# Performance work log

Measured on AMD Instinct MI355X. Metric: run time of the kernel, lower is better.

Reference implementation:

```python
import jax, jax.numpy as jnp
import numpy as np

N, R, B, D, E, P = 100000, 8, 4, 64, 2000000, 500000


def rgcn_conv(x, edge_index, edge_type, comp, basis, root, bias):
    # PyG RGCNConv with basis decomposition and default aggr='mean':
    # per relation r: h_v = mean_{(u->v), type r} x_u ; out_v += h_v @ W_r
    # W_r = sum_b comp[r,b] * basis[b]
    W = jnp.einsum('rb,bio->rio', comp, basis)            # [R, in, out]
    src, dst = edge_index[0], edge_index[1]
    seg = dst * R + edge_type                              # per-(node, relation) segment
    msg = x[src]                                           # [E, in] gather
    sums = jax.ops.segment_sum(msg, seg, num_segments=N * R)
    cnt = jax.ops.segment_sum(jnp.ones((src.shape[0],), x.dtype), seg, num_segments=N * R)
    mean = sums / jnp.maximum(cnt, 1.0)[:, None]           # empty segment -> 0, like PyG
    mean = mean.reshape(N, R, -1)                          # [N, R, in]
    out = jnp.einsum('nri,rio->no', mean, W)
    out = out + x @ root + bias                            # root (self) transform + bias
    return out


def setup_inputs() -> dict:
    key = jax.random.key(0)
    ks = jax.random.split(key, 16)
    s = 0.1
    return {
        'edge_index': jax.random.randint(ks[0], (2, E), 0, N),
        'edge_type': jax.random.randint(ks[1], (E,), 0, R),
        'edge_pairs': jax.random.randint(ks[2], (P, 2), 0, N),
        'node_emb': jax.random.normal(ks[3], (N, D), jnp.float32),
        'comp1': jax.random.normal(ks[4], (R, B), jnp.float32) * s,
        'basis1': jax.random.normal(ks[5], (B, D, D), jnp.float32) * s,
        'root1': jax.random.normal(ks[6], (D, D), jnp.float32) * s,
        'bias1': jnp.zeros((D,), jnp.float32),
        'comp2': jax.random.normal(ks[7], (R, B), jnp.float32) * s,
        'basis2': jax.random.normal(ks[8], (B, D, D), jnp.float32) * s,
        'root2': jax.random.normal(ks[9], (D, D), jnp.float32) * s,
        'bias2': jnp.zeros((D,), jnp.float32),
        'W1': jax.random.normal(ks[10], (2 * D, D), jnp.float32) * s,
        'b1': jnp.zeros((D,), jnp.float32),
        'W2': jax.random.normal(ks[11], (D, 1), jnp.float32) * s,
        'b2': jnp.zeros((1,), jnp.float32),
    }


def reference(edge_index, edge_type, edge_pairs, node_emb, comp1, basis1, root1, bias1,
              comp2, basis2, root2, bias2, W1, b1, W2, b2):
    # encode (eval mode: dropout is identity)
    x = rgcn_conv(node_emb, edge_index, edge_type, comp1, basis1, root1, bias1)
    x = jax.nn.relu(x)
    z = rgcn_conv(x, edge_index, edge_type, comp2, basis2, root2, bias2)
    # decode
    feat = jnp.concatenate([z[edge_pairs[:, 0]], z[edge_pairs[:, 1]]], axis=1)  # [P, 2D]
    h = jax.nn.relu(feat @ W1 + b1)
    logits = (h @ W2 + b2).squeeze(-1)  # [P]
    return logits
```

## Files before the change

kernel.cpp:

```cpp
#include <hip/hip_runtime.h>

constexpr int NN = 100000;
constexpr int RR = 8;
constexpr int BB = 4;
constexpr int DD = 64;
constexpr int EE = 2000000;
constexpr int PP = 500000;
constexpr int CAP = 64;

constexpr int NBIN = 196;
constexpr int BINCAP = 16384;
constexpr int EPB = 4096;

typedef __attribute__((ext_vector_type(8))) short short8;
typedef __attribute__((ext_vector_type(4))) unsigned short ushort4v;
typedef __attribute__((ext_vector_type(4))) float f32x4;

__device__ __forceinline__ unsigned short f2bf(float f) {
    unsigned u = __float_as_uint(f);
    u += 0x7FFFu + ((u >> 16) & 1u);
    return (unsigned short)(u >> 16);
}
__device__ __forceinline__ float bf2f(unsigned short b) {
    return __uint_as_float(((unsigned)b) << 16);
}

__global__ void tobf16_kernel(const float* __restrict__ in, unsigned short* __restrict__ out,
                              int n4) {
    int i = blockIdx.x * blockDim.x + threadIdx.x;
    if (i >= n4) return;
    float4 v = reinterpret_cast<const float4*>(in)[i];
    ushort4v o;
    o.x = f2bf(v.x); o.y = f2bf(v.y); o.z = f2bf(v.z); o.w = f2bf(v.w);
    reinterpret_cast<ushort4v*>(out)[i] = o;
}

__global__ void bin_kernel(const int* __restrict__ src, const int* __restrict__ dst,
                           const int* __restrict__ et, int* __restrict__ bin_cursor,
                           unsigned* __restrict__ ebin) {
    __shared__ int lcount[NBIN];
    __shared__ int lbase[NBIN];
    int tid = threadIdx.x;
    for (int i = tid; i < NBIN; i += 256) lcount[i] = 0;
    __syncthreads();

    int e0 = blockIdx.x * EPB;
    unsigned rec[16];
    int rnk[16];
    int bn[16];
#pragma unroll
    for (int j = 0; j < 16; ++j) {
        int e = e0 + j * 256 + tid;
        if (e < EE) {
            int d = dst[e];
            int b = d >> 9;
            bn[j] = b;
            rec[j] = (unsigned)src[e] | ((unsigned)et[e] << 17) | ((unsigned)(d & 511) << 20);
            rnk[j] = atomicAdd(&lcount[b], 1);
        } else {
            rnk[j] = -1;
        }
    }
    __syncthreads();
    for (int i = tid; i < NBIN; i += 256) lbase[i] = atomicAdd(&bin_cursor[i], lcount[i]);
    __syncthreads();
#pragma unroll
    for (int j = 0; j < 16; ++j) {
        if (rnk[j] >= 0) {
            int pos = lbase[bn[j]] + rnk[j];
            if (pos < BINCAP) ebin[(size_t)bn[j] * BINCAP + pos] = rec[j];
        }
    }
}

__global__ __launch_bounds__(1024) void bucket_kernel(
    const unsigned* __restrict__ ebin, const int* __restrict__ bin_cursor,
    int* __restrict__ cnt, unsigned* __restrict__ epack) {
    __shared__ int lcnt[512];
    int bin = blockIdx.x;
    int tid = threadIdx.x;
    for (int i = tid; i < 512; i += 1024) lcnt[i] = 0;
    __syncthreads();

    int m = bin_cursor[bin];
    if (m > BINCAP) m = BINCAP;
    const unsigned* base = ebin + (size_t)bin * BINCAP;
    int nodebase = bin << 9;

    for (int i = tid; i < m; i += 1024) {
        unsigned rec = base[i];
        int dl = rec >> 20;
        int r = atomicAdd(&lcnt[dl], 1);
        if (r < CAP)
            epack[(size_t)(nodebase + dl) * CAP + r] = rec & 0xFFFFFu;
    }
    __syncthreads();
    for (int i = tid; i < 512; i += 1024) {
        int n = nodebase + i;
        if (n < NN) cnt[n] = lcnt[i];
    }
}

__global__ void aggregate_kernel(const unsigned short* __restrict__ x,
                                 const unsigned* __restrict__ epack,
                                 const int* __restrict__ cnt,
                                 const float* __restrict__ comp,
                                 unsigned short* __restrict__ y) {
    __shared__ float wlds[4 * 32];
    int lane = threadIdx.x & 63;
    int wid = threadIdx.x >> 6;
    int n = blockIdx.x * 4 + wid;
    int half = lane >> 5;
    int fl = lane & 31;

    int m = cnt[n];
    if (m > CAP) m = CAP;

    unsigned pl = (lane < m) ? epack[(size_t)n * CAP + lane] : 0u;
    int et_l = (int)(pl >> 17);

    int cr0 = __popcll(__ballot((lane < m) && (et_l == 0)));
    int cr1 = __popcll(__ballot((lane < m) && (et_l == 1)));
    int cr2 = __popcll(__ballot((lane < m) && (et_l == 2)));
    int cr3 = __popcll(__ballot((lane < m) && (et_l == 3)));
    int cr4 = __popcll(__ballot((lane < m) && (et_l == 4)));
    int cr5 = __popcll(__ballot((lane < m) && (et_l == 5)));
    int cr6 = __popcll(__ballot((lane < m) && (et_l == 6)));
    int cr7 = __popcll(__ballot((lane < m) && (et_l == 7)));

    if (lane < 32) {
        int r = lane >> 2;
        int myc = cr0;
        myc = (r == 1) ? cr1 : myc;
        myc = (r == 2) ? cr2 : myc;
        myc = (r == 3) ? cr3 : myc;
        myc = (r == 4) ? cr4 : myc;
        myc = (r == 5) ? cr5 : myc;
        myc = (r == 6) ? cr6 : myc;
        myc = (r == 7) ? cr7 : myc;
        wlds[wid * 32 + lane] = comp[lane] / fmaxf((float)myc, 1.f);
    }
    __syncthreads();

    float a0x = 0.f, a0y = 0.f, a1x = 0.f, a1y = 0.f;
    float a2x = 0.f, a2y = 0.f, a3x = 0.f, a3y = 0.f;

    int k = 0;
    for (; k + 4 <= m; k += 4) {
        unsigned pA = __shfl(pl, k + half);
        unsigned pB = __shfl(pl, k + 2 + half);
        unsigned rA = *reinterpret_cast<const unsigned*>(
            x + (size_t)(pA & 0x1FFFFu) * 64 + fl * 2);
        unsigned rB = *reinterpret_cast<const unsigned*>(
            x + (size_t)(pB & 0x1FFFFu) * 64 + fl * 2);
        float4 wA = *reinterpret_cast<const float4*>(&wlds[wid * 32 + (pA >> 17) * 4]);
        float4 wB = *reinterpret_cast<const float4*>(&wlds[wid * 32 + (pB >> 17) * 4]);
        float rAx = bf2f((unsigned short)(rA & 0xFFFF));
        float rAy = bf2f((unsigned short)(rA >> 16));
        float rBx = bf2f((unsigned short)(rB & 0xFFFF));
        float rBy = bf2f((unsigned short)(rB >> 16));
        a0x = fmaf(wA.x, rAx, a0x); a0y = fmaf(wA.x, rAy, a0y);
        a1x = fmaf(wA.y, rAx, a1x); a1y = fmaf(wA.y, rAy, a1y);
        a2x = fmaf(wA.z, rAx, a2x); a2y = fmaf(wA.z, rAy, a2y);
        a3x = fmaf(wA.w, rAx, a3x); a3y = fmaf(wA.w, rAy, a3y);
        a0x = fmaf(wB.x, rBx, a0x); a0y = fmaf(wB.x, rBy, a0y);
        a1x = fmaf(wB.y, rBx, a1x); a1y = fmaf(wB.y, rBy, a1y);
        a2x = fmaf(wB.z, rBx, a2x); a2y = fmaf(wB.z, rBy, a2y);
        a3x = fmaf(wB.w, rBx, a3x); a3y = fmaf(wB.w, rBy, a3y);
    }
    for (; k < m; k += 2) {
        int ki = k + half;
        int kc = (ki < m) ? ki : k;
        float sc = (ki < m) ? 1.f : 0.f;
        unsigned p = __shfl(pl, kc);
        unsigned rv = *reinterpret_cast<const unsigned*>(
            x + (size_t)(p & 0x1FFFFu) * 64 + fl * 2);
        float4 wv = *reinterpret_cast<const float4*>(&wlds[wid * 32 + (p >> 17) * 4]);
        float rx = bf2f((unsigned short)(rv & 0xFFFF)) * sc;
        float ry = bf2f((unsigned short)(rv >> 16)) * sc;
        a0x = fmaf(wv.x, rx, a0x); a0y = fmaf(wv.x, ry, a0y);
        a1x = fmaf(wv.y, rx, a1x); a1y = fmaf(wv.y, ry, a1y);
        a2x = fmaf(wv.z, rx, a2x); a2y = fmaf(wv.z, ry, a2y);
        a3x = fmaf(wv.w, rx, a3x); a3y = fmaf(wv.w, ry, a3y);
    }

    a0x += __shfl_xor(a0x, 32); a0y += __shfl_xor(a0y, 32);
    a1x += __shfl_xor(a1x, 32); a1y += __shfl_xor(a1y, 32);
    a2x += __shfl_xor(a2x, 32); a2y += __shfl_xor(a2y, 32);
    a3x += __shfl_xor(a3x, 32); a3y += __shfl_xor(a3y, 32);

    float sLx = half ? a2x : a0x, sLy = half ? a2y : a0y;
    float sHx = half ? a3x : a1x, sHy = half ? a3y : a1y;
    unsigned* y32 = reinterpret_cast<unsigned*>(y + (size_t)n * 256);
    unsigned pL = (unsigned)f2bf(sLx) | ((unsigned)f2bf(sLy) << 16);
    unsigned pH = (unsigned)f2bf(sHx) | ((unsigned)f2bf(sHy) << 16);
    y32[(half * 2) * 32 + fl] = pL;
    y32[(half * 2 + 1) * 32 + fl] = pH;
}


__device__ __forceinline__ void stage_a_f32(const float* __restrict__ src, int blockM, int tid,
                                            unsigned short* Ah, unsigned short* Al) {
#pragma unroll
    for (int j = 0; j < 4; ++j) {
        int e4 = j * 256 + tid;
        int r = e4 >> 4;
        int c4 = (e4 & 15) << 2;
        int gr = blockM + r;
        if (gr > NN - 1) gr = NN - 1;
        float4 v = *reinterpret_cast<const float4*>(src + (size_t)gr * 64 + c4);
        ushort4v hv, lv;
        hv.x = f2bf(v.x); hv.y = f2bf(v.y); hv.z = f2bf(v.z); hv.w = f2bf(v.w);
        lv.x = f2bf(v.x - bf2f(hv.x));
        lv.y = f2bf(v.y - bf2f(hv.y));
        lv.z = f2bf(v.z - bf2f(hv.z));
        lv.w = f2bf(v.w - bf2f(hv.w));
        *reinterpret_cast<ushort4v*>(&Ah[r * 72 + c4]) = hv;
        *reinterpret_cast<ushort4v*>(&Al[r * 72 + c4]) = lv;
    }
}

__device__ __forceinline__ void stage_a_bf(const unsigned short* __restrict__ src,
                                           long rowstride, int blockM, int tid,
                                           unsigned short* A) {
#pragma unroll
    for (int j = 0; j < 4; ++j) {
        int e4 = j * 256 + tid;
        int r = e4 >> 4;
        int c4 = (e4 & 15) << 2;
        int gr = blockM + r;
        if (gr > NN - 1) gr = NN - 1;
        ushort4v v = *reinterpret_cast<const ushort4v*>(src + (size_t)gr * rowstride + c4);
        *reinterpret_cast<ushort4v*>(&A[r * 72 + c4]) = v;
    }
}

__device__ __forceinline__ void stage_b(const float* __restrict__ src, int tid,
                                        unsigned short* Bh, unsigned short* Bl) {
#pragma unroll
    for (int j = 0; j < 4; ++j) {
        int e4 = j * 256 + tid;
        int r = e4 >> 4;
        int c4 = (e4 & 15) << 2;
        float4 v = *reinterpret_cast<const float4*>(src + r * 64 + c4);
        unsigned short h0 = f2bf(v.x), h1 = f2bf(v.y), h2 = f2bf(v.z), h3 = f2bf(v.w);
        Bh[(c4 + 0) * 72 + r] = h0;
        Bh[(c4 + 1) * 72 + r] = h1;
        Bh[(c4 + 2) * 72 + r] = h2;
        Bh[(c4 + 3) * 72 + r] = h3;
        Bl[(c4 + 0) * 72 + r] = f2bf(v.x - bf2f(h0));
        Bl[(c4 + 1) * 72 + r] = f2bf(v.y - bf2f(h1));
        Bl[(c4 + 2) * 72 + r] = f2bf(v.z - bf2f(h2));
        Bl[(c4 + 3) * 72 + r] = f2bf(v.w - bf2f(h3));
    }
}

#define MFMA_CHUNK(ACC)                                                          \
    {                                                                            \
        short8 ah0 = *reinterpret_cast<const short8*>(&Ah[arow * 72 + kb]);      \
        short8 ah1 = *reinterpret_cast<const short8*>(&Ah[arow * 72 + 32 + kb]); \
        short8 al0 = *reinterpret_cast<const short8*>(&Al[arow * 72 + kb]);      \
        short8 al1 = *reinterpret_cast<const short8*>(&Al[arow * 72 + 32 + kb]); \
        _Pragma("unroll")                                                        \
        for (int t = 0; t < 4; ++t) {                                            \
            int bc = t * 16 + ln15;                                              \
            short8 bh0 = *reinterpret_cast<const short8*>(&Bh[bc * 72 + kb]);    \
            short8 bh1 = *reinterpret_cast<const short8*>(&Bh[bc * 72 + 32 + kb]);\
            short8 bl0 = *reinterpret_cast<const short8*>(&Bl[bc * 72 + kb]);    \
            short8 bl1 = *reinterpret_cast<const short8*>(&Bl[bc * 72 + 32 + kb]);\
            ACC[t] = __builtin_amdgcn_mfma_f32_16x16x32_bf16(ah0, bh0, ACC[t], 0, 0, 0); \
            ACC[t] = __builtin_amdgcn_mfma_f32_16x16x32_bf16(ah1, bh1, ACC[t], 0, 0, 0); \
            ACC[t] = __builtin_amdgcn_mfma_f32_16x16x32_bf16(ah0, bl0, ACC[t], 0, 0, 0); \
            ACC[t] = __builtin_amdgcn_mfma_f32_16x16x32_bf16(ah1, bl1, ACC[t], 0, 0, 0); \
            ACC[t] = __builtin_amdgcn_mfma_f32_16x16x32_bf16(al0, bh0, ACC[t], 0, 0, 0); \
            ACC[t] = __builtin_amdgcn_mfma_f32_16x16x32_bf16(al1, bh1, ACC[t], 0, 0, 0); \
        }                                                                        \
    }

#define MFMA_CHUNK_HI(ACC)                                                       \
    {                                                                            \
        short8 ah0 = *reinterpret_cast<const short8*>(&Ah[arow * 72 + kb]);      \
        short8 ah1 = *reinterpret_cast<const short8*>(&Ah[arow * 72 + 32 + kb]); \
        _Pragma("unroll")                                                        \
        for (int t = 0; t < 4; ++t) {                                            \
            int bc = t * 16 + ln15;                                              \
            short8 bh0 = *reinterpret_cast<const short8*>(&Bh[bc * 72 + kb]);    \
            short8 bh1 = *reinterpret_cast<const short8*>(&Bh[bc * 72 + 32 + kb]);\
            short8 bl0 = *reinterpret_cast<const short8*>(&Bl[bc * 72 + kb]);    \
            short8 bl1 = *reinterpret_cast<const short8*>(&Bl[bc * 72 + 32 + kb]);\
            ACC[t] = __builtin_amdgcn_mfma_f32_16x16x32_bf16(ah0, bh0, ACC[t], 0, 0, 0); \
            ACC[t] = __builtin_amdgcn_mfma_f32_16x16x32_bf16(ah1, bh1, ACC[t], 0, 0, 0); \
            ACC[t] = __builtin_amdgcn_mfma_f32_16x16x32_bf16(ah0, bl0, ACC[t], 0, 0, 0); \
            ACC[t] = __builtin_amdgcn_mfma_f32_16x16x32_bf16(ah1, bl1, ACC[t], 0, 0, 0); \
        }                                                                        \
    }

template <int RELU, int PROJ, int XSPLIT>
__global__ __launch_bounds__(256) void combine_mfma(
    const float* __restrict__ xin, const unsigned short* __restrict__ xh,
    const unsigned short* __restrict__ xl, const unsigned short* __restrict__ y,
    const float* __restrict__ basis, const float* __restrict__ root,
    const float* __restrict__ bias, const float* __restrict__ W1,
    unsigned short* __restrict__ o1, unsigned short* __restrict__ o2) {
    __shared__ unsigned short Ah[64 * 72], Al[64 * 72], Bh[64 * 72], Bl[64 * 72];
    int tid = threadIdx.x;
    int lane = tid & 63;
    int wid = tid >> 6;
    int ln15 = lane & 15;
    int blockM = blockIdx.x * 64;
    int wr = wid * 16;
    int arow = wr + ln15;
    int kb = (lane >> 4) * 8;

    f32x4 acc[4];
#pragma unroll
    for (int t = 0; t < 4; ++t) {
        float bv = bias[t * 16 + ln15];
        acc[t] = (f32x4){bv, bv, bv, bv};
    }

    if (XSPLIT) {
        stage_a_bf(xh, 64, blockM, tid, Ah);
        stage_a_bf(xl, 64, blockM, tid, Al);
    } else {
        stage_a_f32(xin, blockM, tid, Ah, Al);
    }
    stage_b(root, tid, Bh, Bl);
    __syncthreads();
    MFMA_CHUNK(acc)

    for (int c = 0; c < 4; ++c) {
        __syncthreads();
        stage_a_bf(y + c * 64, 256, blockM, tid, Ah);
        stage_b(basis + (size_t)c * 4096, tid, Bh, Bl);
        __syncthreads();
        MFMA_CHUNK_HI(acc)
    }

    if (!PROJ) {
#pragma unroll
        for (int t = 0; t < 4; ++t) {
            int cc = t * 16 + ln15;
#pragma unroll
            for (int i = 0; i < 4; ++i) {
                int gr = blockM + wr + (lane >> 4) * 4 + i;
                if (gr < NN) {
                    float v = acc[t][i];
                    if (RELU) v = fmaxf(v, 0.f);
                    unsigned short h = f2bf(v);
                    o1[(size_t)gr * 64 + cc] = h;
                    o2[(size_t)gr * 64 + cc] = f2bf(v - bf2f(h));
                }
            }
        }
    } else {
#pragma unroll
        for (int t = 0; t < 4; ++t) {
            int cc = t * 16 + ln15;
#pragma unroll
            for (int i = 0; i < 4; ++i) {
                int r = wr + (lane >> 4) * 4 + i;
                float v = acc[t][i];
                unsigned short h = f2bf(v);
                Ah[r * 72 + cc] = h;
                Al[r * 72 + cc] = f2bf(v - bf2f(h));
            }
        }
        __syncthreads();
        stage_b(W1, tid, Bh, Bl);
        __syncthreads();
        f32x4 acc2[4];
#pragma unroll
        for (int t = 0; t < 4; ++t) acc2[t] = (f32x4){0.f, 0.f, 0.f, 0.f};
        MFMA_CHUNK(acc2)
#pragma unroll
        for (int t = 0; t < 4; ++t) {
            int cc = t * 16 + ln15;
#pragma unroll
            for (int i = 0; i < 4; ++i) {
                int gr = blockM + wr + (lane >> 4) * 4 + i;
                if (gr < NN) o1[(size_t)gr * 64 + cc] = f2bf(acc2[t][i]);
            }
        }
        __syncthreads();
        stage_b(W1 + 64 * 64, tid, Bh, Bl);
        __syncthreads();
#pragma unroll
        for (int t = 0; t < 4; ++t) acc2[t] = (f32x4){0.f, 0.f, 0.f, 0.f};
        MFMA_CHUNK(acc2)
#pragma unroll
        for (int t = 0; t < 4; ++t) {
            int cc = t * 16 + ln15;
#pragma unroll
            for (int i = 0; i < 4; ++i) {
                int gr = blockM + wr + (lane >> 4) * 4 + i;
                if (gr < NN) o2[(size_t)gr * 64 + cc] = f2bf(acc2[t][i]);
            }
        }
    }
}

__global__ void decode_kernel(const int* __restrict__ pairs,
                              const unsigned short* __restrict__ ha,
                              const unsigned short* __restrict__ hb,
                              const float* __restrict__ b1, const float* __restrict__ W2,
                              const float* __restrict__ b2, float* __restrict__ out) {
    int lane = threadIdx.x & 63;
    int wid = threadIdx.x >> 6;
    int wpair0 = (blockIdx.x * 4 + wid) * 8;
    int pg = lane >> 3;
    int fg = lane & 7;

    int pv = 0;
    if (lane < 16) pv = pairs[(size_t)wpair0 * 2 + lane];
    int a = __shfl(pv, pg * 2);
    int b = __shfl(pv, pg * 2 + 1);

    const float4* b1p = reinterpret_cast<const float4*>(b1 + fg * 8);
    float4 b1a = b1p[0], b1b = b1p[1];
    const float4* w2p = reinterpret_cast<const float4*>(W2 + fg * 8);
    float4 w2a = w2p[0], w2b = w2p[1];

    uint4 hau = *reinterpret_cast<const uint4*>(ha + (size_t)a * 64 + fg * 8);
    uint4 hbu = *reinterpret_cast<const uint4*>(hb + (size_t)b * 64 + fg * 8);

    float s = 0.f;
    s += fmaxf(bf2f((unsigned short)(hau.x & 0xFFFF)) + bf2f((unsigned short)(hbu.x & 0xFFFF)) + b1a.x, 0.f) * w2a.x;
    s += fmaxf(bf2f((unsigned short)(hau.x >> 16))    + bf2f((unsigned short)(hbu.x >> 16))    + b1a.y, 0.f) * w2a.y;
    s += fmaxf(bf2f((unsigned short)(hau.y & 0xFFFF)) + bf2f((unsigned short)(hbu.y & 0xFFFF)) + b1a.z, 0.f) * w2a.z;
    s += fmaxf(bf2f((unsigned short)(hau.y >> 16))    + bf2f((unsigned short)(hbu.y >> 16))    + b1a.w, 0.f) * w2a.w;
    s += fmaxf(bf2f((unsigned short)(hau.z & 0xFFFF)) + bf2f((unsigned short)(hbu.z & 0xFFFF)) + b1b.x, 0.f) * w2b.x;
    s += fmaxf(bf2f((unsigned short)(hau.z >> 16))    + bf2f((unsigned short)(hbu.z >> 16))    + b1b.y, 0.f) * w2b.y;
    s += fmaxf(bf2f((unsigned short)(hau.w & 0xFFFF)) + bf2f((unsigned short)(hbu.w & 0xFFFF)) + b1b.z, 0.f) * w2b.z;
    s += fmaxf(bf2f((unsigned short)(hau.w >> 16))    + bf2f((unsigned short)(hbu.w >> 16))    + b1b.w, 0.f) * w2b.w;

    s += __shfl_xor(s, 1);
    s += __shfl_xor(s, 2);
    s += __shfl_xor(s, 4);
    if (fg == 0) out[wpair0 + pg] = s + b2[0];
}

static inline char* align64(char* p) {
    return (char*)(((uintptr_t)p + 63) & ~(uintptr_t)63);
}

extern "C" void kernel_launch(void* const* d_in, const int* in_sizes, int n_in,
                              void* d_out, int out_size, void* d_ws, size_t ws_size,
                              hipStream_t stream) {
    const int* edge_index = (const int*)d_in[0];
    const int* edge_type  = (const int*)d_in[1];
    const int* edge_pairs = (const int*)d_in[2];
    const float* node_emb = (const float*)d_in[3];
    const float* comp1 = (const float*)d_in[4];
    const float* basis1 = (const float*)d_in[5];
    const float* root1 = (const float*)d_in[6];
    const float* bias1 = (const float*)d_in[7];
    const float* comp2 = (const float*)d_in[8];
    const float* basis2 = (const float*)d_in[9];
    const float* root2 = (const float*)d_in[10];
    const float* bias2 = (const float*)d_in[11];
    const float* W1 = (const float*)d_in[12];
    const float* b1 = (const float*)d_in[13];
    const float* W2 = (const float*)d_in[14];
    const float* b2 = (const float*)d_in[15];

    const int* src = edge_index;
    const int* dst = edge_index + EE;

    char* w = (char*)d_ws;
    int* bin_cursor = (int*)w;            w = align64(w + sizeof(int) * NBIN);
    int* cnt        = (int*)w;            w = align64(w + sizeof(int) * NN);
    unsigned* ebin  = (unsigned*)w;       w = align64(w + sizeof(unsigned) * (size_t)NBIN * BINCAP);
    unsigned* epack = (unsigned*)w;       w = align64(w + sizeof(unsigned) * (size_t)NN * CAP);
    unsigned short* xemb = (unsigned short*)w; w = align64(w + sizeof(short) * (size_t)NN * 64);
    unsigned short* y    = (unsigned short*)w; w = align64(w + sizeof(short) * (size_t)NN * 256);
    unsigned short* x1h  = (unsigned short*)w; w = align64(w + sizeof(short) * (size_t)NN * 64);
    unsigned short* x1l  = (unsigned short*)w; w = align64(w + sizeof(short) * (size_t)NN * 64);
    unsigned short* hab  = (unsigned short*)w; w = align64(w + sizeof(short) * (size_t)NN * 64);
    unsigned short* hbb  = (unsigned short*)w; w = align64(w + sizeof(short) * (size_t)NN * 64);

    hipMemsetAsync(bin_cursor, 0, sizeof(int) * NBIN, stream);
    bin_kernel<<<(EE + EPB - 1) / EPB, 256, 0, stream>>>(src, dst, edge_type, bin_cursor, ebin);
    bucket_kernel<<<NBIN, 1024, 0, stream>>>(ebin, bin_cursor, cnt, epack);
    tobf16_kernel<<<(NN * 16 + 255) / 256, 256, 0, stream>>>(node_emb, xemb, NN * 16);

    aggregate_kernel<<<NN / 4, 256, 0, stream>>>(xemb, epack, cnt, comp1, y);
    combine_mfma<1, 0, 0><<<(NN + 63) / 64, 256, 0, stream>>>(
        node_emb, nullptr, nullptr, y, basis1, root1, bias1, nullptr, x1h, x1l);

    aggregate_kernel<<<NN / 4, 256, 0, stream>>>(x1h, epack, cnt, comp2, y);
    combine_mfma<0, 1, 1><<<(NN + 63) / 64, 256, 0, stream>>>(
        nullptr, x1h, x1l, y, basis2, root2, bias2, W1, hab, hbb);

    decode_kernel<<<PP / 32, 256, 0, stream>>>(edge_pairs, hab, hbb, b1, W2, b2, (float*)d_out);
}
```

Baseline: 335.9 us.

## Fuse neighbor aggregation into the MFMA combine kernel via shared-memory staging

```diff
diff --git a/kernel.cpp b/kernel.cpp
--- a/kernel.cpp
+++ b/kernel.cpp
@@ -12,6 +12,8 @@
 constexpr int BINCAP = 16384;
 constexpr int EPB = 4096;
 
+constexpr int YSTRIDE = 264;
+
 typedef __attribute__((ext_vector_type(8))) short short8;
 typedef __attribute__((ext_vector_type(4))) unsigned short ushort4v;
 typedef __attribute__((ext_vector_type(4))) float f32x4;
@@ -23,6 +25,19 @@
 }
 __device__ __forceinline__ float bf2f(unsigned short b) {
     return __uint_as_float(((unsigned)b) << 16);
+}
+
+__device__ __forceinline__ void split8(const float* __restrict__ p, short8& h, short8& l) {
+    float4 a = *reinterpret_cast<const float4*>(p);
+    float4 b = *reinterpret_cast<const float4*>(p + 4);
+    unsigned short h0 = f2bf(a.x), h1 = f2bf(a.y), h2 = f2bf(a.z), h3 = f2bf(a.w);
+    unsigned short h4 = f2bf(b.x), h5 = f2bf(b.y), h6 = f2bf(b.z), h7 = f2bf(b.w);
+    h = (short8){(short)h0, (short)h1, (short)h2, (short)h3,
+                 (short)h4, (short)h5, (short)h6, (short)h7};
+    l = (short8){(short)f2bf(a.x - bf2f(h0)), (short)f2bf(a.y - bf2f(h1)),
+                 (short)f2bf(a.z - bf2f(h2)), (short)f2bf(a.w - bf2f(h3)),
+                 (short)f2bf(b.x - bf2f(h4)), (short)f2bf(b.y - bf2f(h5)),
+                 (short)f2bf(b.z - bf2f(h6)), (short)f2bf(b.w - bf2f(h7))};
 }
 
 __global__ void tobf16_kernel(const float* __restrict__ in, unsigned short* __restrict__ out,
@@ -98,140 +113,6 @@
     for (int i = tid; i < 512; i += 1024) {
         int n = nodebase + i;
         if (n < NN) cnt[n] = lcnt[i];
-    }
-}
-
-__global__ void aggregate_kernel(const unsigned short* __restrict__ x,
-                                 const unsigned* __restrict__ epack,
-                                 const int* __restrict__ cnt,
-                                 const float* __restrict__ comp,
-                                 unsigned short* __restrict__ y) {
-    __shared__ float wlds[4 * 32];
-    int lane = threadIdx.x & 63;
-    int wid = threadIdx.x >> 6;
-    int n = blockIdx.x * 4 + wid;
-    int half = lane >> 5;
-    int fl = lane & 31;
-
-    int m = cnt[n];
-    if (m > CAP) m = CAP;
-
-    unsigned pl = (lane < m) ? epack[(size_t)n * CAP + lane] : 0u;
-    int et_l = (int)(pl >> 17);
-
-    int cr0 = __popcll(__ballot((lane < m) && (et_l == 0)));
-    int cr1 = __popcll(__ballot((lane < m) && (et_l == 1)));
-    int cr2 = __popcll(__ballot((lane < m) && (et_l == 2)));
-    int cr3 = __popcll(__ballot((lane < m) && (et_l == 3)));
-    int cr4 = __popcll(__ballot((lane < m) && (et_l == 4)));
-    int cr5 = __popcll(__ballot((lane < m) && (et_l == 5)));
-    int cr6 = __popcll(__ballot((lane < m) && (et_l == 6)));
-    int cr7 = __popcll(__ballot((lane < m) && (et_l == 7)));
-
-    if (lane < 32) {
-        int r = lane >> 2;
-        int myc = cr0;
-        myc = (r == 1) ? cr1 : myc;
-        myc = (r == 2) ? cr2 : myc;
-        myc = (r == 3) ? cr3 : myc;
-        myc = (r == 4) ? cr4 : myc;
-        myc = (r == 5) ? cr5 : myc;
-        myc = (r == 6) ? cr6 : myc;
-        myc = (r == 7) ? cr7 : myc;
-        wlds[wid * 32 + lane] = comp[lane] / fmaxf((float)myc, 1.f);
-    }
-    __syncthreads();
-
-    float a0x = 0.f, a0y = 0.f, a1x = 0.f, a1y = 0.f;
-    float a2x = 0.f, a2y = 0.f, a3x = 0.f, a3y = 0.f;
-
-    int k = 0;
-    for (; k + 4 <= m; k += 4) {
-        unsigned pA = __shfl(pl, k + half);
-        unsigned pB = __shfl(pl, k + 2 + half);
-        unsigned rA = *reinterpret_cast<const unsigned*>(
-            x + (size_t)(pA & 0x1FFFFu) * 64 + fl * 2);
-        unsigned rB = *reinterpret_cast<const unsigned*>(
-            x + (size_t)(pB & 0x1FFFFu) * 64 + fl * 2);
-        float4 wA = *reinterpret_cast<const float4*>(&wlds[wid * 32 + (pA >> 17) * 4]);
-        float4 wB = *reinterpret_cast<const float4*>(&wlds[wid * 32 + (pB >> 17) * 4]);
-        float rAx = bf2f((unsigned short)(rA & 0xFFFF));
-        float rAy = bf2f((unsigned short)(rA >> 16));
-        float rBx = bf2f((unsigned short)(rB & 0xFFFF));
-        float rBy = bf2f((unsigned short)(rB >> 16));
-        a0x = fmaf(wA.x, rAx, a0x); a0y = fmaf(wA.x, rAy, a0y);
-        a1x = fmaf(wA.y, rAx, a1x); a1y = fmaf(wA.y, rAy, a1y);
-        a2x = fmaf(wA.z, rAx, a2x); a2y = fmaf(wA.z, rAy, a2y);
-        a3x = fmaf(wA.w, rAx, a3x); a3y = fmaf(wA.w, rAy, a3y);
-        a0x = fmaf(wB.x, rBx, a0x); a0y = fmaf(wB.x, rBy, a0y);
-        a1x = fmaf(wB.y, rBx, a1x); a1y = fmaf(wB.y, rBy, a1y);
-        a2x = fmaf(wB.z, rBx, a2x); a2y = fmaf(wB.z, rBy, a2y);
-        a3x = fmaf(wB.w, rBx, a3x); a3y = fmaf(wB.w, rBy, a3y);
-    }
-    for (; k < m; k += 2) {
-        int ki = k + half;
-        int kc = (ki < m) ? ki : k;
-        float sc = (ki < m) ? 1.f : 0.f;
-        unsigned p = __shfl(pl, kc);
-        unsigned rv = *reinterpret_cast<const unsigned*>(
-            x + (size_t)(p & 0x1FFFFu) * 64 + fl * 2);
-        float4 wv = *reinterpret_cast<const float4*>(&wlds[wid * 32 + (p >> 17) * 4]);
-        float rx = bf2f((unsigned short)(rv & 0xFFFF)) * sc;
-        float ry = bf2f((unsigned short)(rv >> 16)) * sc;
-        a0x = fmaf(wv.x, rx, a0x); a0y = fmaf(wv.x, ry, a0y);
-        a1x = fmaf(wv.y, rx, a1x); a1y = fmaf(wv.y, ry, a1y);
-        a2x = fmaf(wv.z, rx, a2x); a2y = fmaf(wv.z, ry, a2y);
-        a3x = fmaf(wv.w, rx, a3x); a3y = fmaf(wv.w, ry, a3y);
-    }
-
-    a0x += __shfl_xor(a0x, 32); a0y += __shfl_xor(a0y, 32);
-    a1x += __shfl_xor(a1x, 32); a1y += __shfl_xor(a1y, 32);
-    a2x += __shfl_xor(a2x, 32); a2y += __shfl_xor(a2y, 32);
-    a3x += __shfl_xor(a3x, 32); a3y += __shfl_xor(a3y, 32);
-
-    float sLx = half ? a2x : a0x, sLy = half ? a2y : a0y;
-    float sHx = half ? a3x : a1x, sHy = half ? a3y : a1y;
-    unsigned* y32 = reinterpret_cast<unsigned*>(y + (size_t)n * 256);
-    unsigned pL = (unsigned)f2bf(sLx) | ((unsigned)f2bf(sLy) << 16);
-    unsigned pH = (unsigned)f2bf(sHx) | ((unsigned)f2bf(sHy) << 16);
-    y32[(half * 2) * 32 + fl] = pL;
-    y32[(half * 2 + 1) * 32 + fl] = pH;
-}
-
-
-__device__ __forceinline__ void stage_a_f32(const float* __restrict__ src, int blockM, int tid,
-                                            unsigned short* Ah, unsigned short* Al) {
-#pragma unroll
-    for (int j = 0; j < 4; ++j) {
-        int e4 = j * 256 + tid;
-        int r = e4 >> 4;
-        int c4 = (e4 & 15) << 2;
-        int gr = blockM + r;
-        if (gr > NN - 1) gr = NN - 1;
-        float4 v = *reinterpret_cast<const float4*>(src + (size_t)gr * 64 + c4);
-        ushort4v hv, lv;
-        hv.x = f2bf(v.x); hv.y = f2bf(v.y); hv.z = f2bf(v.z); hv.w = f2bf(v.w);
-        lv.x = f2bf(v.x - bf2f(hv.x));
-        lv.y = f2bf(v.y - bf2f(hv.y));
-        lv.z = f2bf(v.z - bf2f(hv.z));
-        lv.w = f2bf(v.w - bf2f(hv.w));
-        *reinterpret_cast<ushort4v*>(&Ah[r * 72 + c4]) = hv;
-        *reinterpret_cast<ushort4v*>(&Al[r * 72 + c4]) = lv;
-    }
-}
-
-__device__ __forceinline__ void stage_a_bf(const unsigned short* __restrict__ src,
-                                           long rowstride, int blockM, int tid,
-                                           unsigned short* A) {
-#pragma unroll
-    for (int j = 0; j < 4; ++j) {
-        int e4 = j * 256 + tid;
-        int r = e4 >> 4;
-        int c4 = (e4 & 15) << 2;
-        int gr = blockM + r;
-        if (gr > NN - 1) gr = NN - 1;
-        ushort4v v = *reinterpret_cast<const ushort4v*>(src + (size_t)gr * rowstride + c4);
-        *reinterpret_cast<ushort4v*>(&A[r * 72 + c4]) = v;
     }
 }
 
@@ -255,12 +136,8 @@
     }
 }
 
-#define MFMA_CHUNK(ACC)                                                          \
+#define MFMA_X(AH0, AH1, AL0, AL1, ACC)                                          \
     {                                                                            \
-        short8 ah0 = *reinterpret_cast<const short8*>(&Ah[arow * 72 + kb]);      \
-        short8 ah1 = *reinterpret_cast<const short8*>(&Ah[arow * 72 + 32 + kb]); \
-        short8 al0 = *reinterpret_cast<const short8*>(&Al[arow * 72 + kb]);      \
-        short8 al1 = *reinterpret_cast<const short8*>(&Al[arow * 72 + 32 + kb]); \
         _Pragma("unroll")                                                        \
         for (int t = 0; t < 4; ++t) {                                            \
             int bc = t * 16 + ln15;                                              \
@@ -268,19 +145,19 @@
             short8 bh1 = *reinterpret_cast<const short8*>(&Bh[bc * 72 + 32 + kb]);\
             short8 bl0 = *reinterpret_cast<const short8*>(&Bl[bc * 72 + kb]);    \
             short8 bl1 = *reinterpret_cast<const short8*>(&Bl[bc * 72 + 32 + kb]);\
-            ACC[t] = __builtin_amdgcn_mfma_f32_16x16x32_bf16(ah0, bh0, ACC[t], 0, 0, 0); \
-            ACC[t] = __builtin_amdgcn_mfma_f32_16x16x32_bf16(ah1, bh1, ACC[t], 0, 0, 0); \
-            ACC[t] = __builtin_amdgcn_mfma_f32_16x16x32_bf16(ah0, bl0, ACC[t], 0, 0, 0); \
-            ACC[t] = __builtin_amdgcn_mfma_f32_16x16x32_bf16(ah1, bl1, ACC[t], 0, 0, 0); \
-            ACC[t] = __builtin_amdgcn_mfma_f32_16x16x32_bf16(al0, bh0, ACC[t], 0, 0, 0); \
-            ACC[t] = __builtin_amdgcn_mfma_f32_16x16x32_bf16(al1, bh1, ACC[t], 0, 0, 0); \
+            ACC[t] = __builtin_amdgcn_mfma_f32_16x16x32_bf16(AH0, bh0, ACC[t], 0, 0, 0); \
+            ACC[t] = __builtin_amdgcn_mfma_f32_16x16x32_bf16(AH1, bh1, ACC[t], 0, 0, 0); \
+            ACC[t] = __builtin_amdgcn_mfma_f32_16x16x32_bf16(AH0, bl0, ACC[t], 0, 0, 0); \
+            ACC[t] = __builtin_amdgcn_mfma_f32_16x16x32_bf16(AH1, bl1, ACC[t], 0, 0, 0); \
+            ACC[t] = __builtin_amdgcn_mfma_f32_16x16x32_bf16(AL0, bh0, ACC[t], 0, 0, 0); \
+            ACC[t] = __builtin_amdgcn_mfma_f32_16x16x32_bf16(AL1, bh1, ACC[t], 0, 0, 0); \
         }                                                                        \
     }
 
-#define MFMA_CHUNK_HI(ACC)                                                       \
+#define MFMA_Y(C, ACC)                                                           \
     {                                                                            \
-        short8 ah0 = *reinterpret_cast<const short8*>(&Ah[arow * 72 + kb]);      \
-        short8 ah1 = *reinterpret_cast<const short8*>(&Ah[arow * 72 + 32 + kb]); \
+        short8 ah0 = *reinterpret_cast<const short8*>(&ys[arow * YSTRIDE + (C) * 64 + kb]);      \
+        short8 ah1 = *reinterpret_cast<const short8*>(&ys[arow * YSTRIDE + (C) * 64 + 32 + kb]); \
         _Pragma("unroll")                                                        \
         for (int t = 0; t < 4; ++t) {                                            \
             int bc = t * 16 + ln15;                                              \
@@ -295,14 +172,29 @@
         }                                                                        \
     }
 
+#define MFMA_Z(ACC)                                                              \
+    {                                                                            \
+        short8 ah0 = *reinterpret_cast<const short8*>(&Zh[arow * 72 + kb]);      \
+        short8 ah1 = *reinterpret_cast<const short8*>(&Zh[arow * 72 + 32 + kb]); \
+        short8 al0 = *reinterpret_cast<const short8*>(&Zl[arow * 72 + kb]);      \
+        short8 al1 = *reinterpret_cast<const short8*>(&Zl[arow * 72 + 32 + kb]); \
+        MFMA_X(ah0, ah1, al0, al1, ACC)                                          \
+    }
+
 template <int RELU, int PROJ, int XSPLIT>
-__global__ __launch_bounds__(256) void combine_mfma(
-    const float* __restrict__ xin, const unsigned short* __restrict__ xh,
-    const unsigned short* __restrict__ xl, const unsigned short* __restrict__ y,
-    const float* __restrict__ basis, const float* __restrict__ root,
-    const float* __restrict__ bias, const float* __restrict__ W1,
+__global__ __launch_bounds__(256) void rgcn_layer(
+    const unsigned short* __restrict__ xg,
+    const float* __restrict__ xf,
+    const unsigned short* __restrict__ xh, const unsigned short* __restrict__ xl,
+    const unsigned* __restrict__ epack, const int* __restrict__ cnt,
+    const float* __restrict__ comp, const float* __restrict__ basis,
+    const float* __restrict__ root, const float* __restrict__ bias,
+    const float* __restrict__ W1,
     unsigned short* __restrict__ o1, unsigned short* __restrict__ o2) {
-    __shared__ unsigned short Ah[64 * 72], Al[64 * 72], Bh[64 * 72], Bl[64 * 72];
+    __shared__ unsigned short ys[64 * YSTRIDE];
+    __shared__ unsigned short Bh[64 * 72], Bl[64 * 72];
+    __shared__ float wlds[4 * 32];
+
     int tid = threadIdx.x;
     int lane = tid & 63;
     int wid = tid >> 6;
@@ -311,6 +203,114 @@
     int wr = wid * 16;
     int arow = wr + ln15;
     int kb = (lane >> 4) * 8;
+    int half = lane >> 5;
+    int fl = lane & 31;
+
+    stage_b(root, tid, Bh, Bl);
+
+    unsigned* ys32 = reinterpret_cast<unsigned*>(ys);
+    for (int j = 0; j < 16; ++j) {
+        int nl = wr + j;
+        int n = blockM + nl;
+        int m = (n < NN) ? cnt[n] : 0;
+        if (m > CAP) m = CAP;
+
+        unsigned pl = (lane < m) ? epack[(size_t)n * CAP + lane] : 0u;
+        int et_l = (int)(pl >> 17);
+
+        int cr0 = __popcll(__ballot((lane < m) && (et_l == 0)));
+        int cr1 = __popcll(__ballot((lane < m) && (et_l == 1)));
+        int cr2 = __popcll(__ballot((lane < m) && (et_l == 2)));
+        int cr3 = __popcll(__ballot((lane < m) && (et_l == 3)));
+        int cr4 = __popcll(__ballot((lane < m) && (et_l == 4)));
+        int cr5 = __popcll(__ballot((lane < m) && (et_l == 5)));
+        int cr6 = __popcll(__ballot((lane < m) && (et_l == 6)));
+        int cr7 = __popcll(__ballot((lane < m) && (et_l == 7)));
+
+        if (lane < 32) {
+            int r = lane >> 2;
+            int myc = cr0;
+            myc = (r == 1) ? cr1 : myc;
+            myc = (r == 2) ? cr2 : myc;
+            myc = (r == 3) ? cr3 : myc;
+            myc = (r == 4) ? cr4 : myc;
+            myc = (r == 5) ? cr5 : myc;
+            myc = (r == 6) ? cr6 : myc;
+            myc = (r == 7) ? cr7 : myc;
+            wlds[wid * 32 + lane] = comp[lane] / fmaxf((float)myc, 1.f);
+        }
+
+        float a0x = 0.f, a0y = 0.f, a1x = 0.f, a1y = 0.f;
+        float a2x = 0.f, a2y = 0.f, a3x = 0.f, a3y = 0.f;
+
+        int k = 0;
+        for (; k + 4 <= m; k += 4) {
+            unsigned pA = __shfl(pl, k + half);
+            unsigned pB = __shfl(pl, k + 2 + half);
+            unsigned rA = *reinterpret_cast<const unsigned*>(
+                xg + (size_t)(pA & 0x1FFFFu) * 64 + fl * 2);
+            unsigned rB = *reinterpret_cast<const unsigned*>(
+                xg + (size_t)(pB & 0x1FFFFu) * 64 + fl * 2);
+            float4 wA = *reinterpret_cast<const float4*>(&wlds[wid * 32 + (pA >> 17) * 4]);
+            float4 wB = *reinterpret_cast<const float4*>(&wlds[wid * 32 + (pB >> 17) * 4]);
+            float rAx = bf2f((unsigned short)(rA & 0xFFFF));
+            float rAy = bf2f((unsigned short)(rA >> 16));
+            float rBx = bf2f((unsigned short)(rB & 0xFFFF));
+            float rBy = bf2f((unsigned short)(rB >> 16));
+            a0x = fmaf(wA.x, rAx, a0x); a0y = fmaf(wA.x, rAy, a0y);
+            a1x = fmaf(wA.y, rAx, a1x); a1y = fmaf(wA.y, rAy, a1y);
+            a2x = fmaf(wA.z, rAx, a2x); a2y = fmaf(wA.z, rAy, a2y);
+            a3x = fmaf(wA.w, rAx, a3x); a3y = fmaf(wA.w, rAy, a3y);
+            a0x = fmaf(wB.x, rBx, a0x); a0y = fmaf(wB.x, rBy, a0y);
+            a1x = fmaf(wB.y, rBx, a1x); a1y = fmaf(wB.y, rBy, a1y);
+            a2x = fmaf(wB.z, rBx, a2x); a2y = fmaf(wB.z, rBy, a2y);
+            a3x = fmaf(wB.w, rBx, a3x); a3y = fmaf(wB.w, rBy, a3y);
+        }
+        for (; k < m; k += 2) {
+            int ki = k + half;
+            int kc = (ki < m) ? ki : k;
+            float sc = (ki < m) ? 1.f : 0.f;
+            unsigned p = __shfl(pl, kc);
+            unsigned rv = *reinterpret_cast<const unsigned*>(
+                xg + (size_t)(p & 0x1FFFFu) * 64 + fl * 2);
+            float4 wv = *reinterpret_cast<const float4*>(&wlds[wid * 32 + (p >> 17) * 4]);
+            float rx = bf2f((unsigned short)(rv & 0xFFFF)) * sc;
+            float ry = bf2f((unsigned short)(rv >> 16)) * sc;
+            a0x = fmaf(wv.x, rx, a0x); a0y = fmaf(wv.x, ry, a0y);
+            a1x = fmaf(wv.y, rx, a1x); a1y = fmaf(wv.y, ry, a1y);
+            a2x = fmaf(wv.z, rx, a2x); a2y = fmaf(wv.z, ry, a2y);
+            a3x = fmaf(wv.w, rx, a3x); a3y = fmaf(wv.w, ry, a3y);
+        }
+
+        a0x += __shfl_xor(a0x, 32); a0y += __shfl_xor(a0y, 32);
+        a1x += __shfl_xor(a1x, 32); a1y += __shfl_xor(a1y, 32);
+        a2x += __shfl_xor(a2x, 32); a2y += __shfl_xor(a2y, 32);
+        a3x += __shfl_xor(a3x, 32); a3y += __shfl_xor(a3y, 32);
+
+        float sLx = half ? a2x : a0x, sLy = half ? a2y : a0y;
+        float sHx = half ? a3x : a1x, sHy = half ? a3y : a1y;
+        unsigned pL = (unsigned)f2bf(sLx) | ((unsigned)f2bf(sLy) << 16);
+        unsigned pH = (unsigned)f2bf(sHx) | ((unsigned)f2bf(sHy) << 16);
+        ys32[nl * (YSTRIDE / 2) + (half * 2) * 32 + fl] = pL;
+        ys32[nl * (YSTRIDE / 2) + (half * 2 + 1) * 32 + fl] = pH;
+    }
+
+    short8 xh0, xh1, xl0, xl1;
+    {
+        int gr = blockM + arow;
+        if (gr > NN - 1) gr = NN - 1;
+        if (XSPLIT) {
+            xh0 = *reinterpret_cast<const short8*>(xh + (size_t)gr * 64 + kb);
+            xh1 = *reinterpret_cast<const short8*>(xh + (size_t)gr * 64 + 32 + kb);
+            xl0 = *reinterpret_cast<const short8*>(xl + (size_t)gr * 64 + kb);
+            xl1 = *reinterpret_cast<const short8*>(xl + (size_t)gr * 64 + 32 + kb);
+        } else {
+            split8(xf + (size_t)gr * 64 + kb, xh0, xl0);
+            split8(xf + (size_t)gr * 64 + 32 + kb, xh1, xl1);
+        }
+    }
+
+    __syncthreads();
 
     f32x4 acc[4];
 #pragma unroll
@@ -319,22 +319,14 @@
         acc[t] = (f32x4){bv, bv, bv, bv};
     }
 
-    if (XSPLIT) {
-        stage_a_bf(xh, 64, blockM, tid, Ah);
-        stage_a_bf(xl, 64, blockM, tid, Al);
-    } else {
-        stage_a_f32(xin, blockM, tid, Ah, Al);
-    }
-    stage_b(root, tid, Bh, Bl);
-    __syncthreads();
-    MFMA_CHUNK(acc)
-
+    MFMA_X(xh0, xh1, xl0, xl1, acc)
+
+#pragma unroll
     for (int c = 0; c < 4; ++c) {
         __syncthreads();
-        stage_a_bf(y + c * 64, 256, blockM, tid, Ah);
         stage_b(basis + (size_t)c * 4096, tid, Bh, Bl);
         __syncthreads();
-        MFMA_CHUNK_HI(acc)
+        MFMA_Y(c, acc)
     }
 
     if (!PROJ) {
@@ -354,6 +346,9 @@
             }
         }
     } else {
+        unsigned short* Zh = ys;
+        unsigned short* Zl = ys + 64 * 72;
+        __syncthreads();
 #pragma unroll
         for (int t = 0; t < 4; ++t) {
             int cc = t * 16 + ln15;
@@ -362,17 +357,16 @@
                 int r = wr + (lane >> 4) * 4 + i;
                 float v = acc[t][i];
                 unsigned short h = f2bf(v);
-                Ah[r * 72 + cc] = h;
-                Al[r * 72 + cc] = f2bf(v - bf2f(h));
+                Zh[r * 72 + cc] = h;
+                Zl[r * 72 + cc] = f2bf(v - bf2f(h));
             }
         }
-        __syncthreads();
         stage_b(W1, tid, Bh, Bl);
         __syncthreads();
         f32x4 acc2[4];
 #pragma unroll
         for (int t = 0; t < 4; ++t) acc2[t] = (f32x4){0.f, 0.f, 0.f, 0.f};
-        MFMA_CHUNK(acc2)
+        MFMA_Z(acc2)
 #pragma unroll
         for (int t = 0; t < 4; ++t) {
             int cc = t * 16 + ln15;
@@ -387,7 +381,7 @@
         __syncthreads();
 #pragma unroll
         for (int t = 0; t < 4; ++t) acc2[t] = (f32x4){0.f, 0.f, 0.f, 0.f};
-        MFMA_CHUNK(acc2)
+        MFMA_Z(acc2)
 #pragma unroll
         for (int t = 0; t < 4; ++t) {
             int cc = t * 16 + ln15;
@@ -473,7 +467,6 @@
     unsigned* ebin  = (unsigned*)w;       w = align64(w + sizeof(unsigned) * (size_t)NBIN * BINCAP);
     unsigned* epack = (unsigned*)w;       w = align64(w + sizeof(unsigned) * (size_t)NN * CAP);
     unsigned short* xemb = (unsigned short*)w; w = align64(w + sizeof(short) * (size_t)NN * 64);
-    unsigned short* y    = (unsigned short*)w; w = align64(w + sizeof(short) * (size_t)NN * 256);
     unsigned short* x1h  = (unsigned short*)w; w = align64(w + sizeof(short) * (size_t)NN * 64);
     unsigned short* x1l  = (unsigned short*)w; w = align64(w + sizeof(short) * (size_t)NN * 64);
     unsigned short* hab  = (unsigned short*)w; w = align64(w + sizeof(short) * (size_t)NN * 64);
@@ -484,13 +477,13 @@
     bucket_kernel<<<NBIN, 1024, 0, stream>>>(ebin, bin_cursor, cnt, epack);
     tobf16_kernel<<<(NN * 16 + 255) / 256, 256, 0, stream>>>(node_emb, xemb, NN * 16);
 
-    aggregate_kernel<<<NN / 4, 256, 0, stream>>>(xemb, epack, cnt, comp1, y);
-    combine_mfma<1, 0, 0><<<(NN + 63) / 64, 256, 0, stream>>>(
-        node_emb, nullptr, nullptr, y, basis1, root1, bias1, nullptr, x1h, x1l);
-
-    aggregate_kernel<<<NN / 4, 256, 0, stream>>>(x1h, epack, cnt, comp2, y);
-    combine_mfma<0, 1, 1><<<(NN + 63) / 64, 256, 0, stream>>>(
-        nullptr, x1h, x1l, y, basis2, root2, bias2, W1, hab, hbb);
+    rgcn_layer<1, 0, 0><<<(NN + 63) / 64, 256, 0, stream>>>(
+        xemb, node_emb, nullptr, nullptr, epack, cnt, comp1, basis1, root1, bias1,
+        nullptr, x1h, x1l);
+
+    rgcn_layer<0, 1, 1><<<(NN + 63) / 64, 256, 0, stream>>>(
+        x1h, nullptr, x1h, x1l, epack, cnt, comp2, basis2, root2, bias2,
+        W1, hab, hbb);
 
     decode_kernel<<<PP / 32, 256, 0, stream>>>(edge_pairs, hab, hbb, b1, W2, b2, (float*)d_out);
 }
```

Measured after the change: 492.5 us. +46.6%, slower.
